# Kernel tuning notes

Measured on AMD Instinct MI355X. Metric: run time of the kernel, lower is better.

## Reference

```python
import jax, jax.numpy as jnp
import numpy as np

N, E, D, H, C = 50000, 800000, 64, 2, 64


def setup_inputs() -> dict:
    key = jax.random.key(0)
    ks = jax.random.split(key, 16)
    sc = 1.0 / np.sqrt(D)
    return {
        "left_features": jax.random.normal(ks[0], (N, D), jnp.float32),
        "edge_index": jax.random.randint(ks[1], (2, E), 0, N, jnp.int32),
        "edge_features": jax.random.normal(ks[2], (E, D), jnp.float32),
        "right_features": jax.random.normal(ks[3], (N, D), jnp.float32),
        "scatter_out_size": N,
        # GATConv params (shared lin for src/dst since in_channels is int)
        "W_lin": jax.random.normal(ks[4], (D, H * C), jnp.float32) * sc,
        "att_src": jax.random.normal(ks[5], (H, C), jnp.float32) * sc,
        "att_dst": jax.random.normal(ks[6], (H, C), jnp.float32) * sc,
        "W_edge": jax.random.normal(ks[7], (D, H * C), jnp.float32) * sc,
        "att_edge": jax.random.normal(ks[8], (H, C), jnp.float32) * sc,
        "bias_conv": jnp.zeros((H * C,), jnp.float32),
        # trailing dense layers
        "W_lt": jax.random.normal(ks[9], (H * C, C), jnp.float32) * sc,
        "b_lt": jnp.zeros((C,), jnp.float32),
        "W_fm": jax.random.normal(ks[10], (C, C), jnp.float32) * sc,
        "b_fm": jnp.zeros((C,), jnp.float32),
        "W_pc": jax.random.normal(ks[11], (2 * C, C), jnp.float32) * sc,
        "b_pc": jnp.zeros((C,), jnp.float32),
    }


def reference(left_features, edge_index, edge_features, right_features,
              scatter_out_size, W_lin, att_src, att_dst, W_edge, att_edge,
              bias_conv, W_lt, b_lt, W_fm, b_fm, W_pc, b_pc):
    src, dst = edge_index[0], edge_index[1]
    Nl = scatter_out_size
    # linear projections to [*, H, C]
    x_src = (right_features @ W_lin).reshape(-1, H, C)
    x_dst = (left_features @ W_lin).reshape(-1, H, C)
    # per-node attention logits [*, H]
    a_src = (x_src * att_src).sum(-1)
    a_dst = (x_dst * att_dst).sum(-1)
    e_feat = (edge_features @ W_edge).reshape(-1, H, C)
    a_edge = (e_feat * att_edge).sum(-1)  # [E, H]
    # per-edge logits, leaky relu, segment softmax over dst neighborhoods
    alpha = a_src[src] + a_dst[dst] + a_edge  # [E, H]
    alpha = jax.nn.leaky_relu(alpha, negative_slope=0.2)
    m = jax.ops.segment_max(alpha, dst, num_segments=Nl)
    m = jnp.where(jnp.isfinite(m), m, 0.0)  # empty segments -> 0
    ex = jnp.exp(alpha - m[dst])
    s = jax.ops.segment_sum(ex, dst, num_segments=Nl)
    att = ex / (s[dst] + 1e-16)  # [E, H]
    # weighted message scatter-sum, concat heads
    msg = x_src[src] * att[:, :, None]  # [E, H, C]
    out = jax.ops.segment_sum(msg, dst, num_segments=Nl).reshape(Nl, H * C)
    out = out + bias_conv
    # trailing dense chain
    x = jax.nn.relu(out) @ W_lt + b_lt          # linear_transform
    x = jax.nn.relu(x) @ W_fm + b_fm            # feature_module_final
    left_updated = jnp.concatenate([left_features, x], axis=-1) @ W_pc + b_pc
    return left_updated, edge_index, att
```

## Files before the change

kernel.cpp:

```cpp
#include <hip/hip_runtime.h>
#include <hip/hip_bf16.h>

typedef unsigned int uint32;
typedef unsigned short ushort16;
typedef float f32x4 __attribute__((ext_vector_type(4)));
typedef short bf16x8 __attribute__((ext_vector_type(8)));

#define HH 2
#define CC 64
#define DD 64
#define HC 128

__device__ __forceinline__ float bf2f(ushort16 u) {
    union { float f; uint32 u; } x; x.u = ((uint32)u) << 16; return x.f;
}
__device__ __forceinline__ ushort16 f2bf(float f) {
    union { float f; uint32 u; } x; x.f = f;
    uint32 u = x.u;
    u += 0x7FFFu + ((u >> 16) & 1u);
    return (ushort16)(u >> 16);
}
__device__ __forceinline__ int clampi(int v, int N) {
    return min(max(v, 0), N - 1);
}
__device__ __forceinline__ float dot4(f32x4 a, f32x4 b) {
    return a.x * b.x + a.y * b.y + a.z * b.z + a.w * b.w;
}
__device__ __forceinline__ void cvt_hilo8(const float* x, bf16x8& hi, bf16x8& lo) {
    #pragma unroll
    for (int i = 0; i < 8; i++) {
        union { float f; uint32 u; } a; a.f = x[i];
        uint32 uh = a.u & 0xFFFF0000u;
        hi[i] = (short)(uh >> 16);
        union { float f; uint32 u; } hf; hf.u = uh;
        lo[i] = (short)f2bf(a.f - hf.f);
    }
}

__global__ void k_fold(const float* W_lin, const float* att_src,
                       const float* att_dst, const float* W_edge,
                       const float* att_edge, float* vfold) {
    int t = threadIdx.x;
    int h = t >> 6, d = t & 63;
    float vs = 0.f, vd = 0.f, ve = 0.f;
    for (int c = 0; c < CC; c++) {
        float wl = W_lin[d * HC + h * CC + c];
        vs += wl * att_src[h * CC + c];
        vd += wl * att_dst[h * CC + c];
        ve += W_edge[d * HC + h * CC + c] * att_edge[h * CC + c];
    }
    vfold[t] = vs; vfold[128 + t] = vd; vfold[256 + t] = ve;
}

__global__ __launch_bounds__(256) void k_node_logits(
    const float* right, const float* left, const float* vfold,
    float* a_src, float* a_dst, int N)
{
    __shared__ float vs[HC], vd[HC];
    if (threadIdx.x < HC) {
        vs[threadIdx.x] = vfold[threadIdx.x];
        vd[threadIdx.x] = vfold[HC + threadIdx.x];
    }
    __syncthreads();
    int g = threadIdx.x >> 4, sub = threadIdx.x & 15;
    f32x4 s0 = *(const f32x4*)&vs[sub * 4];
    f32x4 s1 = *(const f32x4*)&vs[64 + sub * 4];
    f32x4 d0 = *(const f32x4*)&vd[sub * 4];
    f32x4 d1 = *(const f32x4*)&vd[64 + sub * 4];
    #pragma unroll
    for (int it = 0; it < 4; it++) {
        int n = blockIdx.x * 64 + it * 16 + g;
        if (n >= N) break;
        f32x4 r4 = *(const f32x4*)(right + (size_t)n * DD + sub * 4);
        f32x4 l4 = *(const f32x4*)(left  + (size_t)n * DD + sub * 4);
        float p0 = dot4(r4, s0), p1 = dot4(r4, s1);
        float q0 = dot4(l4, d0), q1 = dot4(l4, d1);
        #pragma unroll
        for (int m = 8; m >= 1; m >>= 1) {
            p0 += __shfl_xor(p0, m, 64); p1 += __shfl_xor(p1, m, 64);
            q0 += __shfl_xor(q0, m, 64); q1 += __shfl_xor(q1, m, 64);
        }
        if (sub == 0) {
            *(float2*)(a_src + (size_t)n * 2) = make_float2(p0, p1);
            *(float2*)(a_dst + (size_t)n * 2) = make_float2(q0, q1);
        }
    }
}

__global__ __launch_bounds__(256) void k_edge_alpha(
    const float* edge_feat, const int* ei, const float* vfold,
    const float* a_src, const float* a_dst,
    float* att_slot, int* counts, float* out_ei, int E, int N)
{
    __shared__ float vE[HC];
    if (threadIdx.x < HC) vE[threadIdx.x] = vfold[256 + threadIdx.x];
    __syncthreads();
    int g = threadIdx.x >> 4, sub = threadIdx.x & 15;
    f32x4 w0 = *(const f32x4*)&vE[sub * 4];
    f32x4 w1 = *(const f32x4*)&vE[64 + sub * 4];
    #pragma unroll
    for (int it = 0; it < 4; it++) {
        int e = blockIdx.x * 64 + it * 16 + g;
        if (e >= E) break;
        f32x4 f = *(const f32x4*)(edge_feat + (size_t)e * DD + sub * 4);
        float p0 = dot4(f, w0), p1 = dot4(f, w1);
        #pragma unroll
        for (int m = 8; m >= 1; m >>= 1) {
            p0 += __shfl_xor(p0, m, 64); p1 += __shfl_xor(p1, m, 64);
        }
        if (sub == 0) {
            int raw_s = ei[e], raw_d = ei[E + e];
            int s  = clampi(raw_s, N);
            int d2 = clampi(raw_d, N);
            float2 asr = *(const float2*)(a_src + (size_t)s * 2);
            float2 ads = *(const float2*)(a_dst + (size_t)d2 * 2);
            float al0 = asr.x + ads.x + p0;
            float al1 = asr.y + ads.y + p1;
            al0 = (al0 > 0.f) ? al0 : 0.2f * al0;
            al1 = (al1 > 0.f) ? al1 : 0.2f * al1;
            *(float2*)(att_slot + (size_t)e * 2) = make_float2(al0, al1);
            atomicAdd(&counts[d2], 1);
            out_ei[e]     = (float)raw_s;
            out_ei[E + e] = (float)raw_d;
        }
    }
}

__global__ void k_scan1(const int* counts, int* bsum, int N) {
    int idx = blockIdx.x * 256 + threadIdx.x;
    int v = (idx < N) ? counts[idx] : 0;
    #pragma unroll
    for (int m = 32; m >= 1; m >>= 1) v += __shfl_xor(v, m, 64);
    __shared__ int wsum[4];
    if ((threadIdx.x & 63) == 0) wsum[threadIdx.x >> 6] = v;
    __syncthreads();
    if (threadIdx.x == 0) bsum[blockIdx.x] = wsum[0] + wsum[1] + wsum[2] + wsum[3];
}

__global__ void k_scan2(const int* bsum, int* bpre, int NB) {
    __shared__ int sh[256];
    int t = threadIdx.x;
    int v = (t < NB) ? bsum[t] : 0;
    sh[t] = v;
    __syncthreads();
    for (int off = 1; off < 256; off <<= 1) {
        int add = (t >= off) ? sh[t - off] : 0;
        __syncthreads();
        sh[t] += add;
        __syncthreads();
    }
    if (t < NB) bpre[t] = sh[t] - v;
}

__global__ void k_scan3(const int* counts, const int* bpre,
                        int* offs, int* cursor, int N) {
    __shared__ int sh[256];
    int t = threadIdx.x;
    int idx = blockIdx.x * 256 + t;
    int v = (idx < N) ? counts[idx] : 0;
    sh[t] = v;
    __syncthreads();
    for (int off = 1; off < 256; off <<= 1) {
        int add = (t >= off) ? sh[t - off] : 0;
        __syncthreads();
        sh[t] += add;
        __syncthreads();
    }
    if (idx < N) {
        int ex = bpre[blockIdx.x] + sh[t] - v;
        offs[idx] = ex;
        cursor[idx] = ex;
    }
}

__global__ void k_ids(const int* ei, int* cursor, int* sorted, int E, int N) {
    int e = blockIdx.x * 256 + threadIdx.x;
    if (e >= E) return;
    int d = clampi(ei[E + e], N);
    int pos = atomicAdd(&cursor[d], 1);
    sorted[pos] = e;
}

__global__ __launch_bounds__(256) void k_gather(
    const int* ei, const int* offs, const int* counts, const int* sorted,
    const float* right, float* att_slot, float* agg, int N)
{
    int g = threadIdx.x >> 4, sub = threadIdx.x & 15;
    int n = blockIdx.x * 16 + g;
    if (n >= N) return;
    int start = offs[n], deg = counts[n];
    float m0 = -1e30f, m1 = -1e30f, s0 = 0.f, s1 = 0.f;
    f32x4 acc0 = {0.f, 0.f, 0.f, 0.f}, acc1 = {0.f, 0.f, 0.f, 0.f};
    for (int i = 0; i < deg; i++) {
        int e = sorted[start + i];
        float2 a = *(const float2*)(att_slot + (size_t)e * 2);
        int si = clampi(ei[e], N);
        float nm0 = fmaxf(m0, a.x), nm1 = fmaxf(m1, a.y);
        float f0 = __expf(m0 - nm0), f1 = __expf(m1 - nm1);
        float e0 = __expf(a.x - nm0), e1 = __expf(a.y - nm1);
        f32x4 v = *(const f32x4*)(right + (size_t)si * DD + sub * 4);
        s0 = s0 * f0 + e0;  s1 = s1 * f1 + e1;
        acc0 = acc0 * f0 + e0 * v;
        acc1 = acc1 * f1 + e1 * v;
        m0 = nm0; m1 = nm1;
    }
    float inv0 = 1.f / (s0 + 1e-16f), inv1 = 1.f / (s1 + 1e-16f);
    for (int i = sub; i < deg; i += 16) {
        int e = sorted[start + i];
        float2 a = *(const float2*)(att_slot + (size_t)e * 2);
        a.x = __expf(a.x - m0) * inv0;
        a.y = __expf(a.y - m1) * inv1;
        *(float2*)(att_slot + (size_t)e * 2) = a;
    }
    *(f32x4*)(agg + (size_t)n * HC + sub * 4)      = acc0 * inv0;
    *(f32x4*)(agg + (size_t)n * HC + 64 + sub * 4) = acc1 * inv1;
}

__global__ __launch_bounds__(256) void k_lin_mfma(
    const float* __restrict__ W_lin, const float* __restrict__ bc,
    float* agg, int N)
{
    __shared__ __align__(16) ushort16 sW[16][512];
    __shared__ float sB[HC];
    for (int t = threadIdx.x; t < 16 * 64; t += 256) {
        int lane = t & 63, f = t >> 6;
        int nt = f & 3, kt = (f >> 2) & 1, h = f >> 3;
        int n = h * CC + nt * 16 + (lane & 15);
        int k0 = kt * 32 + (lane >> 4) * 8;
        #pragma unroll
        for (int i = 0; i < 8; i++)
            sW[f][lane * 8 + i] = f2bf(W_lin[(size_t)(k0 + i) * HC + n]);
    }
    if (threadIdx.x < HC) sB[threadIdx.x] = bc[threadIdx.x];
    __syncthreads();
    int w = threadIdx.x >> 6, lane = threadIdx.x & 63;
    int lhi = lane >> 4, llo = lane & 15;
    int tiles = (N + 63) >> 6;
    for (int tile = blockIdx.x; tile < tiles; tile += gridDim.x) {
        int nb = tile * 64 + w * 16;
        int arow = min(nb + llo, N - 1);
        const float* ap = agg + (size_t)arow * HC;
        bf16x8 Ah[2][2], Al[2][2];
        #pragma unroll
        for (int h = 0; h < 2; h++)
            #pragma unroll
            for (int kt = 0; kt < 2; kt++) {
                float x8[8];
                *(f32x4*)&x8[0] = *(const f32x4*)(ap + h * 64 + kt * 32 + lhi * 8);
                *(f32x4*)&x8[4] = *(const f32x4*)(ap + h * 64 + kt * 32 + lhi * 8 + 4);
                cvt_hilo8(x8, Ah[h][kt], Al[h][kt]);
            }
        f32x4 acc[2][4];
        #pragma unroll
        for (int h = 0; h < 2; h++)
            #pragma unroll
            for (int nt = 0; nt < 4; nt++) {
                float b = sB[h * 64 + nt * 16 + llo];
                acc[h][nt][0] = b; acc[h][nt][1] = b;
                acc[h][nt][2] = b; acc[h][nt][3] = b;
            }
        #pragma unroll
        for (int h = 0; h < 2; h++)
            #pragma unroll
            for (int kt = 0; kt < 2; kt++)
                #pragma unroll
                for (int nt = 0; nt < 4; nt++) {
                    bf16x8 b = *(const bf16x8*)&sW[h * 8 + kt * 4 + nt][lane * 8];
                    acc[h][nt] = __builtin_amdgcn_mfma_f32_16x16x32_bf16(Al[h][kt], b, acc[h][nt], 0, 0, 0);
                    acc[h][nt] = __builtin_amdgcn_mfma_f32_16x16x32_bf16(Ah[h][kt], b, acc[h][nt], 0, 0, 0);
                }
        #pragma unroll
        for (int h = 0; h < 2; h++)
            #pragma unroll
            for (int nt = 0; nt < 4; nt++)
                #pragma unroll
                for (int j = 0; j < 4; j++) {
                    int node = nb + 4 * lhi + j;
                    if (node < N)
                        agg[(size_t)node * HC + h * 64 + nt * 16 + llo] =
                            fmaxf(acc[h][nt][j], 0.f);
                }
    }
}

__global__ __launch_bounds__(256) void k_tail_mfma(
    const float* __restrict__ t0, const float* __restrict__ left,
    const float* __restrict__ W_lt, const float* __restrict__ b_lt,
    const float* __restrict__ W_fm, const float* __restrict__ b_fm,
    const float* __restrict__ W_pc, const float* __restrict__ b_pc,
    float* __restrict__ out, int N)
{
    __shared__ __align__(16) ushort16 sWlt[16][512];
    __shared__ __align__(16) ushort16 sWfm[8][512];
    __shared__ __align__(16) ushort16 sWpT[8][512];
    __shared__ __align__(16) ushort16 sWpB[8][512];
    __shared__ __align__(16) float sX[4][1024];
    __shared__ float sblt[CC], sbfm[CC], sbpc[CC];
    for (int t = threadIdx.x; t < 16 * 64; t += 256) {
        int lane = t & 63, f = t >> 6, nt = f & 3, kt = f >> 2;
        int n = nt * 16 + (lane & 15), k0 = kt * 32 + (lane >> 4) * 8;
        #pragma unroll
        for (int i = 0; i < 8; i++)
            sWlt[f][lane * 8 + i] = f2bf(W_lt[(k0 + i) * CC + n]);
    }
    for (int t = threadIdx.x; t < 8 * 64; t += 256) {
        int lane = t & 63, f = t >> 6, nt = f & 3, kt = f >> 2;
        int n = nt * 16 + (lane & 15), k0 = kt * 32 + (lane >> 4) * 8;
        #pragma unroll
        for (int i = 0; i < 8; i++) {
            sWfm[f][lane * 8 + i] = f2bf(W_fm[(k0 + i) * CC + n]);
            sWpT[f][lane * 8 + i] = f2bf(W_pc[(k0 + i) * CC + n]);
            sWpB[f][lane * 8 + i] = f2bf(W_pc[(64 + k0 + i) * CC + n]);
        }
    }
    if (threadIdx.x < CC) {
        sblt[threadIdx.x] = b_lt[threadIdx.x];
        sbfm[threadIdx.x] = b_fm[threadIdx.x];
        sbpc[threadIdx.x] = b_pc[threadIdx.x];
    }
    __syncthreads();
    int w = threadIdx.x >> 6, lane = threadIdx.x & 63;
    int lhi = lane >> 4, llo = lane & 15;
    float* xw = &sX[w][0];
    int swz = (llo & 7) << 2;
    int tiles = (N + 63) >> 6;
    for (int tile = blockIdx.x; tile < tiles; tile += gridDim.x) {
        int nb = tile * 64 + w * 16;
        int arow = min(nb + llo, N - 1);
        f32x4 acc2[4];
        #pragma unroll
        for (int nt = 0; nt < 4; nt++) {
            float b = sblt[nt * 16 + llo];
            acc2[nt][0] = b; acc2[nt][1] = b; acc2[nt][2] = b; acc2[nt][3] = b;
        }
        const float* tp = t0 + (size_t)arow * HC;
        #pragma unroll
        for (int kt = 0; kt < 4; kt++) {
            float x8[8];
            *(f32x4*)&x8[0] = *(const f32x4*)(tp + kt * 32 + lhi * 8);
            *(f32x4*)&x8[4] = *(const f32x4*)(tp + kt * 32 + lhi * 8 + 4);
            bf16x8 ah, al; cvt_hilo8(x8, ah, al);
            #pragma unroll
            for (int nt = 0; nt < 4; nt++) {
                bf16x8 b = *(const bf16x8*)&sWlt[kt * 4 + nt][lane * 8];
                acc2[nt] = __builtin_amdgcn_mfma_f32_16x16x32_bf16(al, b, acc2[nt], 0, 0, 0);
                acc2[nt] = __builtin_amdgcn_mfma_f32_16x16x32_bf16(ah, b, acc2[nt], 0, 0, 0);
            }
        }
        #pragma unroll
        for (int nt = 0; nt < 4; nt++)
            #pragma unroll
            for (int j = 0; j < 4; j++) {
                int row = 4 * lhi + j, col = nt * 16 + llo;
                xw[row * 64 + (col ^ ((row & 7) << 2))] = fmaxf(acc2[nt][j], 0.f);
            }
        f32x4 acc3[4];
        #pragma unroll
        for (int nt = 0; nt < 4; nt++) {
            float b = sbfm[nt * 16 + llo];
            acc3[nt][0] = b; acc3[nt][1] = b; acc3[nt][2] = b; acc3[nt][3] = b;
        }
        #pragma unroll
        for (int kt = 0; kt < 2; kt++) {
            int k0 = kt * 32 + lhi * 8;
            float x8[8];
            *(f32x4*)&x8[0] = *(const f32x4*)&xw[llo * 64 + ((k0    ) ^ swz)];
            *(f32x4*)&x8[4] = *(const f32x4*)&xw[llo * 64 + ((k0 + 4) ^ swz)];
            bf16x8 ah, al; cvt_hilo8(x8, ah, al);
            #pragma unroll
            for (int nt = 0; nt < 4; nt++) {
                bf16x8 b = *(const bf16x8*)&sWfm[kt * 4 + nt][lane * 8];
                acc3[nt] = __builtin_amdgcn_mfma_f32_16x16x32_bf16(al, b, acc3[nt], 0, 0, 0);
                acc3[nt] = __builtin_amdgcn_mfma_f32_16x16x32_bf16(ah, b, acc3[nt], 0, 0, 0);
            }
        }
        #pragma unroll
        for (int nt = 0; nt < 4; nt++)
            #pragma unroll
            for (int j = 0; j < 4; j++) {
                int row = 4 * lhi + j, col = nt * 16 + llo;
                xw[row * 64 + (col ^ ((row & 7) << 2))] = acc3[nt][j];
            }
        f32x4 acc4[4];
        #pragma unroll
        for (int nt = 0; nt < 4; nt++) {
            float b = sbpc[nt * 16 + llo];
            acc4[nt][0] = b; acc4[nt][1] = b; acc4[nt][2] = b; acc4[nt][3] = b;
        }
        const float* lp = left + (size_t)arow * DD;
        #pragma unroll
        for (int kt = 0; kt < 2; kt++) {
            float x8[8];
            *(f32x4*)&x8[0] = *(const f32x4*)(lp + kt * 32 + lhi * 8);
            *(f32x4*)&x8[4] = *(const f32x4*)(lp + kt * 32 + lhi * 8 + 4);
            bf16x8 ah, al; cvt_hilo8(x8, ah, al);
            #pragma unroll
            for (int nt = 0; nt < 4; nt++) {
                bf16x8 b = *(const bf16x8*)&sWpT[kt * 4 + nt][lane * 8];
                acc4[nt] = __builtin_amdgcn_mfma_f32_16x16x32_bf16(al, b, acc4[nt], 0, 0, 0);
                acc4[nt] = __builtin_amdgcn_mfma_f32_16x16x32_bf16(ah, b, acc4[nt], 0, 0, 0);
            }
        }
        #pragma unroll
        for (int kt = 0; kt < 2; kt++) {
            int k0 = kt * 32 + lhi * 8;
            float x8[8];
            *(f32x4*)&x8[0] = *(const f32x4*)&xw[llo * 64 + ((k0    ) ^ swz)];
            *(f32x4*)&x8[4] = *(const f32x4*)&xw[llo * 64 + ((k0 + 4) ^ swz)];
            bf16x8 ah, al; cvt_hilo8(x8, ah, al);
            #pragma unroll
            for (int nt = 0; nt < 4; nt++) {
                bf16x8 b = *(const bf16x8*)&sWpB[kt * 4 + nt][lane * 8];
                acc4[nt] = __builtin_amdgcn_mfma_f32_16x16x32_bf16(al, b, acc4[nt], 0, 0, 0);
                acc4[nt] = __builtin_amdgcn_mfma_f32_16x16x32_bf16(ah, b, acc4[nt], 0, 0, 0);
            }
        }
        #pragma unroll
        for (int nt = 0; nt < 4; nt++)
            #pragma unroll
            for (int j = 0; j < 4; j++) {
                int node = nb + 4 * lhi + j;
                if (node < N)
                    out[(size_t)node * CC + nt * 16 + llo] = acc4[nt][j];
            }
    }
}

extern "C" void kernel_launch(void* const* d_in, const int* in_sizes, int n_in,
                              void* d_out, int out_size, void* d_ws, size_t ws_size,
                              hipStream_t stream) {
    const float* left      = (const float*)d_in[0];
    const int*   ei        = (const int*)d_in[1];
    const float* efeat     = (const float*)d_in[2];
    const float* right     = (const float*)d_in[3];
    const float* W_lin     = (const float*)d_in[5];
    const float* att_src   = (const float*)d_in[6];
    const float* att_dst   = (const float*)d_in[7];
    const float* W_edge    = (const float*)d_in[8];
    const float* att_edge  = (const float*)d_in[9];
    const float* bias_conv = (const float*)d_in[10];
    const float* W_lt      = (const float*)d_in[11];
    const float* b_lt      = (const float*)d_in[12];
    const float* b_fm      = (const float*)d_in[14];
    const float* W_fm      = (const float*)d_in[13];
    const float* W_pc      = (const float*)d_in[15];
    const float* b_pc      = (const float*)d_in[16];

    const int N = in_sizes[0] / DD;
    const int E = in_sizes[2] / DD;
    const int NB = (N + 255) / 256;

    float* ws     = (float*)d_ws;
    float* vfold  = ws;
    float* a_src  = ws + 512;
    float* a_dst  = a_src + 2 * (size_t)N;
    int*   counts = (int*)(a_dst + 2 * (size_t)N);
    int*   offs   = counts + N;
    int*   cursor = offs + N;
    int*   bsum   = cursor + N;
    int*   bpre   = bsum + 256;
    int*   sorted = bpre + 256;
    float* agg    = (float*)(sorted + E);
    (void)ws_size; (void)n_in; (void)out_size;

    float* out_lu   = (float*)d_out;
    float* out_ei   = out_lu + (size_t)N * CC;
    float* att_slot = out_ei + (size_t)2 * E;

    hipMemsetAsync(counts, 0, (size_t)N * sizeof(int), stream);

    hipLaunchKernelGGL(k_fold, dim3(1), dim3(128), 0, stream,
                       W_lin, att_src, att_dst, W_edge, att_edge, vfold);
    hipLaunchKernelGGL(k_node_logits, dim3((N + 63) / 64), dim3(256), 0, stream,
                       right, left, vfold, a_src, a_dst, N);
    hipLaunchKernelGGL(k_edge_alpha, dim3((E + 63) / 64), dim3(256), 0, stream,
                       efeat, ei, vfold, a_src, a_dst, att_slot, counts, out_ei,
                       E, N);
    hipLaunchKernelGGL(k_scan1, dim3(NB), dim3(256), 0, stream,
                       counts, bsum, N);
    hipLaunchKernelGGL(k_scan2, dim3(1), dim3(256), 0, stream,
                       bsum, bpre, NB);
    hipLaunchKernelGGL(k_scan3, dim3(NB), dim3(256), 0, stream,
                       counts, bpre, offs, cursor, N);
    hipLaunchKernelGGL(k_ids, dim3((E + 255) / 256), dim3(256), 0, stream,
                       ei, cursor, sorted, E, N);
    hipLaunchKernelGGL(k_gather, dim3((N + 15) / 16), dim3(256), 0, stream,
                       ei, offs, counts, sorted, right, att_slot, agg, N);
    hipLaunchKernelGGL(k_lin_mfma, dim3(512), dim3(256), 0, stream,
                       W_lin, bias_conv, agg, N);
    hipLaunchKernelGGL(k_tail_mfma, dim3(512), dim3(256), 0, stream,
                       agg, left, W_lt, b_lt, W_fm, b_fm, W_pc, b_pc, out_lu, N);
}
```

Before: 525.8 us.

## Sort edge payload by destination and unroll softmax-aggregate gather by four

The bucket-sort step now writes a packed float4 payload (two logits, source index, edge id) per edge in destination order, instead of only the edge id. The gather kernel then reads it contiguously rather than chasing edge ids into att_slot and edge_index. The gather loop is unrolled by four so several neighbour feature loads are in flight together, using masked duplicate loads for the tail. The edge-index float copy is also moved to a coalesced per-block write, at the cost of a larger workspace and extra scatter traffic in k_ids.

```diff
diff --git a/kernel.cpp b/kernel.cpp
--- a/kernel.cpp
+++ b/kernel.cpp
@@ -109,9 +109,8 @@
             p0 += __shfl_xor(p0, m, 64); p1 += __shfl_xor(p1, m, 64);
         }
         if (sub == 0) {
-            int raw_s = ei[e], raw_d = ei[E + e];
-            int s  = clampi(raw_s, N);
-            int d2 = clampi(raw_d, N);
+            int s  = clampi(ei[e], N);
+            int d2 = clampi(ei[E + e], N);
             float2 asr = *(const float2*)(a_src + (size_t)s * 2);
             float2 ads = *(const float2*)(a_dst + (size_t)d2 * 2);
             float al0 = asr.x + ads.x + p0;
@@ -120,9 +119,15 @@
             al1 = (al1 > 0.f) ? al1 : 0.2f * al1;
             *(float2*)(att_slot + (size_t)e * 2) = make_float2(al0, al1);
             atomicAdd(&counts[d2], 1);
-            out_ei[e]     = (float)raw_s;
-            out_ei[E + e] = (float)raw_d;
-        }
+        }
+    }
+    int t = threadIdx.x, base = blockIdx.x * 64;
+    if (t < 64) {
+        int i = base + t;
+        if (i < E) out_ei[i] = (float)ei[i];
+    } else if (t < 128) {
+        int i = base + (t - 64);
+        if (i < E) out_ei[E + i] = (float)ei[E + i];
     }
 }
 
@@ -173,16 +178,19 @@
     }
 }
 
-__global__ void k_ids(const int* ei, int* cursor, int* sorted, int E, int N) {
+__global__ void k_ids(const int* ei, const float* att_slot, int* cursor,
+                      float4* payload, int E, int N) {
     int e = blockIdx.x * 256 + threadIdx.x;
     if (e >= E) return;
+    int s = clampi(ei[e], N);
     int d = clampi(ei[E + e], N);
+    float2 a = *(const float2*)(att_slot + (size_t)e * 2);
     int pos = atomicAdd(&cursor[d], 1);
-    sorted[pos] = e;
+    payload[pos] = make_float4(a.x, a.y, __int_as_float(s), __int_as_float(e));
 }
 
 __global__ __launch_bounds__(256) void k_gather(
-    const int* ei, const int* offs, const int* counts, const int* sorted,
+    const float4* payload, const int* offs, const int* counts,
     const float* right, float* att_slot, float* agg, int N)
 {
     int g = threadIdx.x >> 4, sub = threadIdx.x & 15;
@@ -191,26 +199,39 @@
     int start = offs[n], deg = counts[n];
     float m0 = -1e30f, m1 = -1e30f, s0 = 0.f, s1 = 0.f;
     f32x4 acc0 = {0.f, 0.f, 0.f, 0.f}, acc1 = {0.f, 0.f, 0.f, 0.f};
-    for (int i = 0; i < deg; i++) {
-        int e = sorted[start + i];
-        float2 a = *(const float2*)(att_slot + (size_t)e * 2);
-        int si = clampi(ei[e], N);
-        float nm0 = fmaxf(m0, a.x), nm1 = fmaxf(m1, a.y);
+    for (int base = 0; base < deg; base += 4) {
+        int last = deg - 1;
+        float4 p0 = payload[start + min(base,     last)];
+        float4 p1 = payload[start + min(base + 1, last)];
+        float4 p2 = payload[start + min(base + 2, last)];
+        float4 p3 = payload[start + min(base + 3, last)];
+        float k1 = (base + 1 < deg) ? 1.f : 0.f;
+        float k2 = (base + 2 < deg) ? 1.f : 0.f;
+        float k3 = (base + 3 < deg) ? 1.f : 0.f;
+        f32x4 v0 = *(const f32x4*)(right + (size_t)__float_as_int(p0.z) * DD + sub * 4);
+        f32x4 v1 = *(const f32x4*)(right + (size_t)__float_as_int(p1.z) * DD + sub * 4);
+        f32x4 v2 = *(const f32x4*)(right + (size_t)__float_as_int(p2.z) * DD + sub * 4);
+        f32x4 v3 = *(const f32x4*)(right + (size_t)__float_as_int(p3.z) * DD + sub * 4);
+        float bm0 = fmaxf(fmaxf(p0.x, p1.x), fmaxf(p2.x, p3.x));
+        float bm1 = fmaxf(fmaxf(p0.y, p1.y), fmaxf(p2.y, p3.y));
+        float nm0 = fmaxf(m0, bm0), nm1 = fmaxf(m1, bm1);
         float f0 = __expf(m0 - nm0), f1 = __expf(m1 - nm1);
-        float e0 = __expf(a.x - nm0), e1 = __expf(a.y - nm1);
-        f32x4 v = *(const f32x4*)(right + (size_t)si * DD + sub * 4);
-        s0 = s0 * f0 + e0;  s1 = s1 * f1 + e1;
-        acc0 = acc0 * f0 + e0 * v;
-        acc1 = acc1 * f1 + e1 * v;
+        float e00 = __expf(p0.x - nm0),      e10 = __expf(p0.y - nm1);
+        float e01 = __expf(p1.x - nm0) * k1, e11 = __expf(p1.y - nm1) * k1;
+        float e02 = __expf(p2.x - nm0) * k2, e12 = __expf(p2.y - nm1) * k2;
+        float e03 = __expf(p3.x - nm0) * k3, e13 = __expf(p3.y - nm1) * k3;
+        s0 = s0 * f0 + (e00 + e01 + e02 + e03);
+        s1 = s1 * f1 + (e10 + e11 + e12 + e13);
+        acc0 = acc0 * f0 + e00 * v0 + e01 * v1 + e02 * v2 + e03 * v3;
+        acc1 = acc1 * f1 + e10 * v0 + e11 * v1 + e12 * v2 + e13 * v3;
         m0 = nm0; m1 = nm1;
     }
     float inv0 = 1.f / (s0 + 1e-16f), inv1 = 1.f / (s1 + 1e-16f);
     for (int i = sub; i < deg; i += 16) {
-        int e = sorted[start + i];
-        float2 a = *(const float2*)(att_slot + (size_t)e * 2);
-        a.x = __expf(a.x - m0) * inv0;
-        a.y = __expf(a.y - m1) * inv1;
-        *(float2*)(att_slot + (size_t)e * 2) = a;
+        float4 p = payload[start + i];
+        int e = __float_as_int(p.w);
+        *(float2*)(att_slot + (size_t)e * 2) =
+            make_float2(__expf(p.x - m0) * inv0, __expf(p.y - m1) * inv1);
     }
     *(f32x4*)(agg + (size_t)n * HC + sub * 4)      = acc0 * inv0;
     *(f32x4*)(agg + (size_t)n * HC + 64 + sub * 4) = acc1 * inv1;
@@ -441,8 +462,8 @@
     const float* bias_conv = (const float*)d_in[10];
     const float* W_lt      = (const float*)d_in[11];
     const float* b_lt      = (const float*)d_in[12];
+    const float* W_fm      = (const float*)d_in[13];
     const float* b_fm      = (const float*)d_in[14];
-    const float* W_fm      = (const float*)d_in[13];
     const float* W_pc      = (const float*)d_in[15];
     const float* b_pc      = (const float*)d_in[16];
 
@@ -459,8 +480,9 @@
     int*   cursor = offs + N;
     int*   bsum   = cursor + N;
     int*   bpre   = bsum + 256;
-    int*   sorted = bpre + 256;
-    float* agg    = (float*)(sorted + E);
+    size_t po     = ((size_t)(1024 + 7 * (size_t)N) + 3) & ~(size_t)3;
+    float4* payload = (float4*)(ws + po);
+    float* agg    = ws + po + 4 * (size_t)E;
     (void)ws_size; (void)n_in; (void)out_size;
 
     float* out_lu   = (float*)d_out;
@@ -483,9 +505,9 @@
     hipLaunchKernelGGL(k_scan3, dim3(NB), dim3(256), 0, stream,
                        counts, bpre, offs, cursor, N);
     hipLaunchKernelGGL(k_ids, dim3((E + 255) / 256), dim3(256), 0, stream,
-                       ei, cursor, sorted, E, N);
+                       ei, att_slot, cursor, payload, E, N);
     hipLaunchKernelGGL(k_gather, dim3((N + 15) / 16), dim3(256), 0, stream,
-                       ei, offs, counts, sorted, right, att_slot, agg, N);
+                       payload, offs, counts, right, att_slot, agg, N);
     hipLaunchKernelGGL(k_lin_mfma, dim3(512), dim3(256), 0, stream,
                        W_lin, bias_conv, agg, N);
     hipLaunchKernelGGL(k_tail_mfma, dim3(512), dim3(256), 0, stream,
```

Measured after the change: 491.0 us. 1.07x faster.
